# Optimization experiments

Hardware: AMD Instinct MI355X
Metric: run time of the kernel (lower is better)

## Reference

```python
import jax, jax.numpy as jnp
import numpy as np

HIDDEN = 2048
N_HEADS = 32
N_KV_HEADS = 8
N_GROUPS = N_HEADS // N_KV_HEADS  # 4
HEAD_DIM = HIDDEN // N_HEADS      # 64
BATCH, SEQ = 2, 2048


def setup_inputs() -> dict:
    key = jax.random.key(0)
    ks = jax.random.split(key, 5)
    s = 0.02
    return {
        "x": jax.random.normal(ks[0], (BATCH, SEQ, HIDDEN), dtype=jnp.float32),
        "Wq": jax.random.normal(ks[1], (HIDDEN, HIDDEN), dtype=jnp.float32) * s,
        "Wk": jax.random.normal(ks[2], (N_KV_HEADS * HEAD_DIM, HIDDEN), dtype=jnp.float32) * s,
        "Wv": jax.random.normal(ks[3], (N_KV_HEADS * HEAD_DIM, HIDDEN), dtype=jnp.float32) * s,
        "Wo": jax.random.normal(ks[4], (HIDDEN, HIDDEN), dtype=jnp.float32) * s,
    }


def reference(x, Wq, Wk, Wv, Wo):
    b, s, _ = x.shape
    # Projections (nn.Linear: y = x @ W.T)
    q = (x @ Wq.T).reshape(b, s, N_KV_HEADS, N_GROUPS, HEAD_DIM)  # group heads by kv head
    k = (x @ Wk.T).reshape(b, s, N_KV_HEADS, HEAD_DIM)
    v = (x @ Wv.T).reshape(b, s, N_KV_HEADS, HEAD_DIM)
    scale = 1.0 / jnp.sqrt(jnp.asarray(HEAD_DIM, dtype=x.dtype))
    # Grouped scores: equivalent to repeat_interleave of K over groups
    scores = jnp.einsum('bqhgd,bkhd->bhgqk', q, k) * scale  # [b, kvh, g, s, s]
    causal_mask = jnp.triu(jnp.ones((s, s), dtype=bool), k=1)
    scores = jnp.where(causal_mask, -jnp.inf, scores)
    attn = jax.nn.softmax(scores, axis=-1)
    out = jnp.einsum('bhgqk,bkhd->bqhgd', attn, v)  # [b, s, kvh, g, hd]
    out = out.reshape(b, s, HIDDEN)
    return out @ Wo.T
```

## Files before the change

### kernel.cpp

```cpp
#include <hip/hip_runtime.h>

#define HIDDEN 2048
#define NHEADS 32
#define NKV 8
#define HD 64
#define BATCH 2
#define SEQ 2048
#define MROWS (BATCH*SEQ)
#define KVDIM (NKV*HD)
#define QKVN (HIDDEN + 2*KVDIM)

typedef __bf16 bf16x8 __attribute__((ext_vector_type(8)));
typedef __bf16 bf16x4 __attribute__((ext_vector_type(4)));
typedef float f32x4 __attribute__((ext_vector_type(4)));

__device__ inline f32x4 mfma32(bf16x8 a, bf16x8 b, f32x4 c) {
    return __builtin_amdgcn_mfma_f32_16x16x32_bf16(a, b, c, 0, 0, 0);
}

__device__ inline void gld16(const __bf16* g, __bf16* l) {
    __builtin_amdgcn_global_load_lds((const __attribute__((address_space(1))) void*)g,
                                     (__attribute__((address_space(3))) void*)l, 16, 0, 0);
}

__global__ __launch_bounds__(256) void cast_all(const float* __restrict__ x,
                                                const float* __restrict__ wq,
                                                const float* __restrict__ wk,
                                                const float* __restrict__ wv,
                                                const float* __restrict__ wo,
                                                __bf16* __restrict__ xb,
                                                __bf16* __restrict__ wqkv,
                                                __bf16* __restrict__ wob,
                                                float qscale) {
    int blk = blockIdx.x;
    const float* src; __bf16* dst; float sc = 1.0f; size_t off;
    if (blk < 8192)        { src = x;  dst = xb;   off = (size_t)blk * 1024; }
    else if (blk < 12288)  { src = wq; dst = wqkv; off = (size_t)(blk - 8192) * 1024; sc = qscale; }
    else if (blk < 13312)  { src = wk; dst = wqkv + (size_t)HIDDEN * HIDDEN; off = (size_t)(blk - 12288) * 1024; }
    else if (blk < 14336)  { src = wv; dst = wqkv + (size_t)(HIDDEN + KVDIM) * HIDDEN; off = (size_t)(blk - 13312) * 1024; }
    else                   { src = wo; dst = wob;  off = (size_t)(blk - 14336) * 1024; }
    size_t i4 = off + (size_t)threadIdx.x * 4;
    float4 f = *(const float4*)(src + i4);
    dst[i4 + 0] = (__bf16)(f.x * sc);
    dst[i4 + 1] = (__bf16)(f.y * sc);
    dst[i4 + 2] = (__bf16)(f.z * sc);
    dst[i4 + 3] = (__bf16)(f.w * sc);
}

__device__ inline void store_val(__bf16* C, size_t idx, float v) { C[idx] = (__bf16)v; }
__device__ inline void store_val(float* C, size_t idx, float v) { C[idx] = v; }

template <typename OutT>
__global__ __launch_bounds__(256) void gemm128(const __bf16* __restrict__ A,
                                               const __bf16* __restrict__ B,
                                               OutT* __restrict__ C,
                                               int M, int N, int K) {
    __shared__ __bf16 As[2][128][32];
    __shared__ __bf16 Bs[2][128][32];
    const int tid  = threadIdx.x;
    const int lane = tid & 63;
    const int w    = tid >> 6;
    const int col  = lane & 15;
    const int quad = lane >> 4;
    const int m0 = blockIdx.y * 128;
    const int n0 = blockIdx.x * 128;
    const int wm = (w >> 1) * 64;
    const int wn = (w & 1) * 64;

    f32x4 acc[4][4];
    #pragma unroll
    for (int i = 0; i < 4; i++)
        #pragma unroll
        for (int j = 0; j < 4; j++) acc[i][j] = (f32x4){0.f,0.f,0.f,0.f};

    const int lrow = lane >> 2;
    const int lcol = (lane & 3) * 8;

    auto stage = [&](int k0, int buf) {
        #pragma unroll
        for (int c = 0; c < 4; c++) {
            int chunk = w * 4 + c;
            if (chunk < 8) {
                const __bf16* g = A + (size_t)(m0 + chunk*16 + lrow) * K + k0 + lcol;
                gld16(g, &As[buf][chunk*16][0]);
            } else {
                int bc = chunk - 8;
                const __bf16* g = B + (size_t)(n0 + bc*16 + lrow) * K + k0 + lcol;
                gld16(g, &Bs[buf][bc*16][0]);
            }
        }
    };

    const int nk = K / 32;
    stage(0, 0);
    for (int ki = 0; ki < nk; ki++) {
        const int buf = ki & 1;
        __syncthreads();
        if (ki + 1 < nk) stage((ki + 1) * 32, buf ^ 1);

        bf16x8 af[4], bfr[4];
        #pragma unroll
        for (int i = 0; i < 4; i++) af[i]  = *(const bf16x8*)&As[buf][wm + i*16 + col][quad*8];
        #pragma unroll
        for (int j = 0; j < 4; j++) bfr[j] = *(const bf16x8*)&Bs[buf][wn + j*16 + col][quad*8];
        #pragma unroll
        for (int i = 0; i < 4; i++)
            #pragma unroll
            for (int j = 0; j < 4; j++)
                acc[i][j] = __builtin_amdgcn_mfma_f32_16x16x32_bf16(af[i], bfr[j], acc[i][j], 0, 0, 0);
    }

    #pragma unroll
    for (int i = 0; i < 4; i++) {
        #pragma unroll
        for (int r = 0; r < 4; r++) {
            int mrow = m0 + wm + i*16 + quad*4 + r;
            size_t base = (size_t)mrow * N + n0 + wn;
            #pragma unroll
            for (int j = 0; j < 4; j++)
                store_val(C, base + j*16 + col, acc[i][j][r]);
        }
    }
}

__global__ __launch_bounds__(512, 2) void gemm256(const __bf16* __restrict__ A,
                                                  const __bf16* __restrict__ B,
                                                  __bf16* __restrict__ C,
                                                  int M, int N, int K) {
    __shared__ __bf16 As[2][256][64];
    __shared__ __bf16 Bs[2][192][64];
    const int tid  = threadIdx.x;
    const int lane = tid & 63;
    const int w    = tid >> 6;
    const int wr   = w >> 2;
    const int wc   = w & 3;
    const int col  = lane & 15;
    const int quad = lane >> 4;
    const int m0 = blockIdx.y * 256;
    const int n0 = blockIdx.x * 192;
    const int nk = K >> 6;

    f32x4 acc[8][3];
    #pragma unroll
    for (int i = 0; i < 8; i++)
        #pragma unroll
        for (int j = 0; j < 3; j++) acc[i][j] = (f32x4){0.f,0.f,0.f,0.f};

    bf16x8 amh0[4][2];
    bf16x8 amh1[4][2];
    bf16x8 b01[2][2];
    bf16x8 b2v[2];

    const int r8 = lane >> 3, c8 = lane & 7;
    const __bf16* pA0 = A + (size_t)(m0 + w*16 +     r8) * K + ((c8 ^ quad) * 8);
    const __bf16* pA1 = A + (size_t)(m0 + w*16 + 8 + r8) * K + ((c8 ^ (4 + quad)) * 8);
    const __bf16* pB  = B + (size_t)(n0 + w*8 +      r8) * K + ((c8 ^ ((w & 1) * 4 + quad)) * 8);
    const int rsw = col >> 1;

    auto issue = [&](int tt) {
        if (tt < nk) {
            int b = tt & 1; size_t ko = (size_t)tt * 64;
            gld16(pA0 + ko,                  &As[b][w*16][0]);
            gld16(pA1 + ko,                  &As[b][w*16 + 8][0]);
            gld16(pA0 + (size_t)128*K + ko,  &As[b][128 + w*16][0]);
            gld16(pA1 + (size_t)128*K + ko,  &As[b][128 + w*16 + 8][0]);
            gld16(pB + ko,                   &Bs[b][w*8][0]);
            gld16(pB + (size_t)64*K + ko,    &Bs[b][64 + w*8][0]);
            gld16(pB + (size_t)128*K + ko,   &Bs[b][128 + w*8][0]);
        }
    };
    auto rdA = [&](bf16x8 (&dst)[4][2], int b, int rowbase) {
        #pragma unroll
        for (int i = 0; i < 4; i++) {
            const __bf16* rp = &As[b][rowbase + i*16 + col][0];
            #pragma unroll
            for (int kk = 0; kk < 2; kk++)
                dst[i][kk] = *(const bf16x8*)(rp + (((kk*4 + quad) ^ rsw) * 8));
        }
    };
    auto rdB01 = [&](int b) {
        #pragma unroll
        for (int j = 0; j < 2; j++) {
            const __bf16* rp = &Bs[b][wc*48 + j*16 + col][0];
            #pragma unroll
            for (int kk = 0; kk < 2; kk++)
                b01[j][kk] = *(const bf16x8*)(rp + (((kk*4 + quad) ^ rsw) * 8));
        }
    };

    issue(0); issue(1);
    __asm__ volatile("s_waitcnt vmcnt(7)" ::: "memory");
    __builtin_amdgcn_s_barrier();
    __asm__ volatile("" ::: "memory");
    rdA(amh0, 0, wr*128);
    rdB01(0);

    for (int t = 0; t < nk; ++t) {
        const int buf = t & 1;
        {
            const __bf16* rp = &Bs[buf][wc*48 + 32 + col][0];
            #pragma unroll
            for (int kk = 0; kk < 2; kk++)
                b2v[kk] = *(const bf16x8*)(rp + (((kk*4 + quad) ^ rsw) * 8));
        }
        __builtin_amdgcn_s_setprio(1);
        #pragma unroll
        for (int i = 0; i < 4; i++)
            #pragma unroll
            for (int j = 0; j < 2; j++)
                #pragma unroll
                for (int kk = 0; kk < 2; kk++)
                    acc[i][j] = mfma32(amh0[i][kk], b01[j][kk], acc[i][j]);
        __builtin_amdgcn_s_setprio(0);
        rdA(amh1, buf, wr*128 + 64);
        __builtin_amdgcn_s_setprio(1);
        #pragma unroll
        for (int i = 0; i < 4; i++)
            #pragma unroll
            for (int kk = 0; kk < 2; kk++)
                acc[i][2] = mfma32(amh0[i][kk], b2v[kk], acc[i][2]);
        __builtin_amdgcn_s_setprio(0);
        __builtin_amdgcn_s_setprio(1);
        #pragma unroll
        for (int i = 0; i < 4; i++)
            #pragma unroll
            for (int j = 0; j < 2; j++)
                #pragma unroll
                for (int kk = 0; kk < 2; kk++)
                    acc[4+i][j] = mfma32(amh1[i][kk], b01[j][kk], acc[4+i][j]);
        __builtin_amdgcn_s_setprio(0);

        __asm__ volatile("s_waitcnt vmcnt(0) lgkmcnt(0)" ::: "memory");
        __builtin_amdgcn_sched_barrier(0);
        __builtin_amdgcn_s_barrier();
        __asm__ volatile("" ::: "memory");

        if (t + 1 < nk) {
            rdA(amh0, buf ^ 1, wr*128);
            rdB01(buf ^ 1);
        }
        issue(t + 2);

        __builtin_amdgcn_s_setprio(1);
        #pragma unroll
        for (int i = 0; i < 4; i++)
            #pragma unroll
            for (int kk = 0; kk < 2; kk++)
                acc[4+i][2] = mfma32(amh1[i][kk], b2v[kk], acc[4+i][2]);
        __builtin_amdgcn_s_setprio(0);
    }

    #pragma unroll
    for (int i16 = 0; i16 < 8; i16++) {
        #pragma unroll
        for (int r = 0; r < 4; r++) {
            size_t base = (size_t)(m0 + wr*128 + i16*16 + quad*4 + r) * N + n0 + wc*48;
            #pragma unroll
            for (int j = 0; j < 3; j++)
                C[base + j*16 + col] = (__bf16)acc[i16][j][r];
        }
    }
}

__global__ __launch_bounds__(256) void transpose_v(const __bf16* __restrict__ QKV,
                                                   __bf16* __restrict__ VT) {
    __shared__ __bf16 tile[64][72];
    const int r0 = blockIdx.x * 64;
    const int s0 = blockIdx.y * 64;
    const int t  = threadIdx.x;
    #pragma unroll
    for (int cc = 0; cc < 2; cc++) {
        int c = t + cc * 256;
        int i = c >> 3;
        int j8 = (c & 7) * 8;
        bf16x8 v = *(const bf16x8*)(QKV + (size_t)(s0 + i) * QKVN + (HIDDEN + KVDIM) + r0 + j8);
        *(bf16x8*)&tile[i][j8] = v;
    }
    __syncthreads();
    #pragma unroll
    for (int cc = 0; cc < 2; cc++) {
        int c = t + cc * 256;
        int d = c >> 3;
        int m = c & 7;
        bf16x8 vv;
        #pragma unroll
        for (int tt = 0; tt < 8; tt++) {
            int sl = (m >> 2) * 32 + (tt >> 2) * 16 + (m & 3) * 4 + (tt & 3);
            vv[tt] = tile[sl][d];
        }
        *(bf16x8*)(VT + (size_t)(r0 + d) * MROWS + s0 + m * 8) = vv;
    }
}

__global__ __launch_bounds__(256) void flash_attn(const __bf16* __restrict__ QKV,
                                                  const __bf16* __restrict__ VT,
                                                  __bf16* __restrict__ O) {
    const int bid  = blockIdx.x;
    const int t    = 31 - (bid >> 6);
    const int head = (bid >> 1) & 31;
    const int b    = bid & 1;
    const int kvh  = head >> 2;
    const int tid  = threadIdx.x;
    const int lane = tid & 63;
    const int w    = tid >> 6;
    const int col  = lane & 15;
    const int quad = lane >> 4;

    const int qb   = t * 64 + w * 16;
    const int n32  = (t + 1) * 2;

    __shared__ __bf16 Ks[3][2][32][32];
    __shared__ __bf16 Vs[3][64][32];

    const size_t qO = (size_t)(b * SEQ + qb + col) * QKVN + head * HD;
    bf16x8 aq0 = *(const bf16x8*)(QKV + qO + quad * 8);
    bf16x8 aq1 = *(const bf16x8*)(QKV + qO + 32 + quad * 8);

    bf16x8 ones8;
    #pragma unroll
    for (int j = 0; j < 8; j++) ones8[j] = (__bf16)1.0f;

    f32x4 o[4];
    #pragma unroll
    for (int dn = 0; dn < 4; dn++) o[dn] = (f32x4){0.f,0.f,0.f,0.f};
    f32x4 lsum = (f32x4){0.f,0.f,0.f,0.f};

    const int lrow = lane >> 2;
    const int srcc8 = (((lane & 3) ^ (lrow & 3)) * 8);
    const int swz   = (quad ^ (col & 3)) * 8;
    const size_t bS = (size_t)b * SEQ;

    const __bf16 *g0, *g1;
    size_t gstep;
    if (w < 2) {
        g0 = QKV + (bS + lrow) * QKVN + HIDDEN + kvh * HD + w * 32 + srcc8;
        g1 = g0 + (size_t)16 * QKVN;
        gstep = (size_t)32 * QKVN;
    } else {
        g0 = VT + (size_t)(kvh * HD + (w - 2) * 32 + lrow) * MROWS + bS + (lane & 3) * 8;
        g1 = g0 + (size_t)16 * MROWS;
        gstep = 32;
    }

    auto stage = [&](int sb) {
        if (w < 2) {
            gld16(g0, &Ks[sb][w][0][0]);
            gld16(g1, &Ks[sb][w][16][0]);
        } else {
            gld16(g0, &Vs[sb][(w - 2) * 32][0]);
            gld16(g1, &Vs[sb][(w - 2) * 32 + 16][0]);
        }
        g0 += gstep; g1 += gstep;
    };

    stage(0);
    stage(1);
    int cur = 0, nx2 = 2;
    for (int kt = 0; kt < n32; kt++) {
        const int kbase = kt * 32;
        if (kt + 1 < n32) { __asm__ volatile("s_waitcnt vmcnt(2)" ::: "memory"); }
        else              { __asm__ volatile("s_waitcnt vmcnt(0)" ::: "memory"); }
        __builtin_amdgcn_s_barrier();
        __asm__ volatile("" ::: "memory");
        if (kt + 2 < n32) stage(nx2);

        f32x4 s[2];
        s[0] = (f32x4){0.f,0.f,0.f,0.f};
        s[1] = (f32x4){0.f,0.f,0.f,0.f};
        __builtin_amdgcn_s_setprio(1);
        #pragma unroll
        for (int j = 0; j < 2; j++) {
            bf16x8 bk0 = *(const bf16x8*)&Ks[cur][0][j*16 + col][swz];
            bf16x8 bk1 = *(const bf16x8*)&Ks[cur][1][j*16 + col][swz];
            s[j] = mfma32(bk0, aq0, s[j]);
            s[j] = mfma32(bk1, aq1, s[j]);
        }
        __builtin_amdgcn_s_setprio(0);

        if (kt >= n32 - 2) {
            #pragma unroll
            for (int j = 0; j < 2; j++)
                #pragma unroll
                for (int r = 0; r < 4; r++)
                    if (kbase + j*16 + quad*4 + r > qb + col) s[j][r] = -1e30f;
        }

        bf16x8 pa;
        #pragma unroll
        for (int j = 0; j < 2; j++)
            #pragma unroll
            for (int r = 0; r < 4; r++)
                pa[j*4 + r] = (__bf16)__builtin_amdgcn_exp2f(s[j][r]);

        __builtin_amdgcn_s_setprio(1);
        lsum = mfma32(pa, ones8, lsum);
        #pragma unroll
        for (int dn = 0; dn < 4; dn++) {
            bf16x8 bv = *(const bf16x8*)&Vs[cur][dn*16 + col][quad*8];
            o[dn] = mfma32(pa, bv, o[dn]);
        }
        __builtin_amdgcn_s_setprio(0);

        cur = (cur == 2) ? 0 : cur + 1;
        nx2 = (nx2 == 2) ? 0 : nx2 + 1;
    }

    #pragma unroll
    for (int r = 0; r < 4; r++) {
        float inv = 1.0f / lsum[r];
        __bf16* op = O + (size_t)(b * SEQ + qb + quad*4 + r) * HIDDEN + head * HD;
        #pragma unroll
        for (int dn = 0; dn < 4; dn++)
            op[dn*16 + col] = (__bf16)(o[dn][r] * inv);
    }
}

extern "C" void kernel_launch(void* const* d_in, const int* in_sizes, int n_in,
                              void* d_out, int out_size, void* d_ws, size_t ws_size,
                              hipStream_t stream) {
    const float* x  = (const float*)d_in[0];
    const float* Wq = (const float*)d_in[1];
    const float* Wk = (const float*)d_in[2];
    const float* Wv = (const float*)d_in[3];
    const float* Wo = (const float*)d_in[4];
    float* out = (float*)d_out;

    __bf16* p    = (__bf16*)d_ws;
    __bf16* xb   = p; p += (size_t)MROWS * HIDDEN;
    __bf16* wqkv = p; p += (size_t)QKVN * HIDDEN;
    __bf16* wob  = p; p += (size_t)HIDDEN * HIDDEN;
    __bf16* qkv  = p; p += (size_t)MROWS * QKVN;
    __bf16* vt   = p; p += (size_t)KVDIM * MROWS;
    __bf16* aob  = xb;

    const float qscale = 0.125f * 1.4426950408889634f;
    cast_all<<<18432, 256, 0, stream>>>(x, Wq, Wk, Wv, Wo, xb, wqkv, wob, qscale);

    gemm256<<<dim3(QKVN/192, MROWS/256), 512, 0, stream>>>(xb, wqkv, qkv, MROWS, QKVN, HIDDEN);
    transpose_v<<<dim3(KVDIM/64, MROWS/64), dim3(256), 0, stream>>>(qkv, vt);
    flash_attn<<<BATCH * NHEADS * (SEQ/64), dim3(256), 0, stream>>>(qkv, vt, aob);
    gemm128<float><<<dim3(HIDDEN/128, MROWS/128), dim3(256), 0, stream>>>(aob, wob, out, MROWS, HIDDEN, HIDDEN);
}
```

Baseline: 271.7 us.

## Double flash-attention query tile to 128 rows with two 16-row subtiles per wave

Each attention block now handles 128 query rows, and each wave computes two 16-row query subtiles against every K/V tile it stages in LDS. This halves the number of blocks and roughly halves the K/V global-to-LDS traffic per query row. A wave skips the MFMA work for its first subtile once that subtile lies entirely under the causal mask. The block-to-tile mapping is reordered to interleave heavy and light causal tiles, and the V tile now uses the same XOR swizzle as K. The cost is more registers per wave and fewer blocks, which may lower occupancy and tail balance.

Result: no change. 275.2 us (+1.3%).

```diff
diff --git a/kernel.cpp b/kernel.cpp
--- a/kernel.cpp
+++ b/kernel.cpp
@@ -296,7 +296,8 @@
                                                   const __bf16* __restrict__ VT,
                                                   __bf16* __restrict__ O) {
     const int bid  = blockIdx.x;
-    const int t    = 31 - (bid >> 6);
+    const int g    = bid >> 6;
+    const int t    = ((g >> 2) & 1) ? ((g & 8) ? (g - 12) : (g + 4)) : (15 - g);
     const int head = (bid >> 1) & 31;
     const int b    = bid & 1;
     const int kvh  = head >> 2;
@@ -306,24 +307,28 @@
     const int col  = lane & 15;
     const int quad = lane >> 4;
 
-    const int qb   = t * 64 + w * 16;
-    const int n32  = (t + 1) * 2;
+    const int qb   = t * 128 + w * 32;
+    const int n32  = (t + 1) * 4;
 
     __shared__ __bf16 Ks[3][2][32][32];
     __shared__ __bf16 Vs[3][64][32];
 
-    const size_t qO = (size_t)(b * SEQ + qb + col) * QKVN + head * HD;
-    bf16x8 aq0 = *(const bf16x8*)(QKV + qO + quad * 8);
-    bf16x8 aq1 = *(const bf16x8*)(QKV + qO + 32 + quad * 8);
+    const size_t qOA = (size_t)(b * SEQ + qb + col) * QKVN + head * HD;
+    const size_t qOB = qOA + (size_t)16 * QKVN;
+    bf16x8 aqA0 = *(const bf16x8*)(QKV + qOA + quad * 8);
+    bf16x8 aqA1 = *(const bf16x8*)(QKV + qOA + 32 + quad * 8);
+    bf16x8 aqB0 = *(const bf16x8*)(QKV + qOB + quad * 8);
+    bf16x8 aqB1 = *(const bf16x8*)(QKV + qOB + 32 + quad * 8);
 
     bf16x8 ones8;
     #pragma unroll
     for (int j = 0; j < 8; j++) ones8[j] = (__bf16)1.0f;
 
-    f32x4 o[4];
-    #pragma unroll
-    for (int dn = 0; dn < 4; dn++) o[dn] = (f32x4){0.f,0.f,0.f,0.f};
-    f32x4 lsum = (f32x4){0.f,0.f,0.f,0.f};
+    f32x4 oA[4], oB[4];
+    #pragma unroll
+    for (int dn = 0; dn < 4; dn++) { oA[dn] = (f32x4){0.f,0.f,0.f,0.f}; oB[dn] = (f32x4){0.f,0.f,0.f,0.f}; }
+    f32x4 lsumA = (f32x4){0.f,0.f,0.f,0.f};
+    f32x4 lsumB = (f32x4){0.f,0.f,0.f,0.f};
 
     const int lrow = lane >> 2;
     const int srcc8 = (((lane & 3) ^ (lrow & 3)) * 8);
@@ -337,7 +342,7 @@
         g1 = g0 + (size_t)16 * QKVN;
         gstep = (size_t)32 * QKVN;
     } else {
-        g0 = VT + (size_t)(kvh * HD + (w - 2) * 32 + lrow) * MROWS + bS + (lane & 3) * 8;
+        g0 = VT + (size_t)(kvh * HD + (w - 2) * 32 + lrow) * MROWS + bS + srcc8;
         g1 = g0 + (size_t)16 * MROWS;
         gstep = 32;
     }
@@ -364,42 +369,67 @@
         __asm__ volatile("" ::: "memory");
         if (kt + 2 < n32) stage(nx2);
 
-        f32x4 s[2];
-        s[0] = (f32x4){0.f,0.f,0.f,0.f};
-        s[1] = (f32x4){0.f,0.f,0.f,0.f};
-        __builtin_amdgcn_s_setprio(1);
-        #pragma unroll
-        for (int j = 0; j < 2; j++) {
-            bf16x8 bk0 = *(const bf16x8*)&Ks[cur][0][j*16 + col][swz];
-            bf16x8 bk1 = *(const bf16x8*)&Ks[cur][1][j*16 + col][swz];
-            s[j] = mfma32(bk0, aq0, s[j]);
-            s[j] = mfma32(bk1, aq1, s[j]);
-        }
-        __builtin_amdgcn_s_setprio(0);
-
-        if (kt >= n32 - 2) {
+        const bool doB = (kbase <= qb + 31);
+        const bool doA = (kbase <= qb + 15);
+
+        if (doB) {
+            f32x4 sA[2], sB[2];
+            #pragma unroll
+            for (int j = 0; j < 2; j++) { sA[j] = (f32x4){0.f,0.f,0.f,0.f}; sB[j] = (f32x4){0.f,0.f,0.f,0.f}; }
+            __builtin_amdgcn_s_setprio(1);
+            #pragma unroll
+            for (int j = 0; j < 2; j++) {
+                bf16x8 bk0 = *(const bf16x8*)&Ks[cur][0][j*16 + col][swz];
+                bf16x8 bk1 = *(const bf16x8*)&Ks[cur][1][j*16 + col][swz];
+                sB[j] = mfma32(bk0, aqB0, sB[j]);
+                sB[j] = mfma32(bk1, aqB1, sB[j]);
+                if (doA) {
+                    sA[j] = mfma32(bk0, aqA0, sA[j]);
+                    sA[j] = mfma32(bk1, aqA1, sA[j]);
+                }
+            }
+            __builtin_amdgcn_s_setprio(0);
+
+            if (kbase + 31 > qb + 16) {
+                #pragma unroll
+                for (int j = 0; j < 2; j++)
+                    #pragma unroll
+                    for (int r = 0; r < 4; r++)
+                        if (kbase + j*16 + quad*4 + r > qb + 16 + col) sB[j][r] = -1e30f;
+            }
+            if (doA && (kbase + 31 > qb)) {
+                #pragma unroll
+                for (int j = 0; j < 2; j++)
+                    #pragma unroll
+                    for (int r = 0; r < 4; r++)
+                        if (kbase + j*16 + quad*4 + r > qb + col) sA[j][r] = -1e30f;
+            }
+
+            bf16x8 paB, paA;
             #pragma unroll
             for (int j = 0; j < 2; j++)
                 #pragma unroll
                 for (int r = 0; r < 4; r++)
-                    if (kbase + j*16 + quad*4 + r > qb + col) s[j][r] = -1e30f;
-        }
-
-        bf16x8 pa;
-        #pragma unroll
-        for (int j = 0; j < 2; j++)
-            #pragma unroll
-            for (int r = 0; r < 4; r++)
-                pa[j*4 + r] = (__bf16)__builtin_amdgcn_exp2f(s[j][r]);
-
-        __builtin_amdgcn_s_setprio(1);
-        lsum = mfma32(pa, ones8, lsum);
-        #pragma unroll
-        for (int dn = 0; dn < 4; dn++) {
-            bf16x8 bv = *(const bf16x8*)&Vs[cur][dn*16 + col][quad*8];
-            o[dn] = mfma32(pa, bv, o[dn]);
-        }
-        __builtin_amdgcn_s_setprio(0);
+                    paB[j*4 + r] = (__bf16)__builtin_amdgcn_exp2f(sB[j][r]);
+            if (doA) {
+                #pragma unroll
+                for (int j = 0; j < 2; j++)
+                    #pragma unroll
+                    for (int r = 0; r < 4; r++)
+                        paA[j*4 + r] = (__bf16)__builtin_amdgcn_exp2f(sA[j][r]);
+            }
+
+            __builtin_amdgcn_s_setprio(1);
+            lsumB = mfma32(paB, ones8, lsumB);
+            if (doA) lsumA = mfma32(paA, ones8, lsumA);
+            #pragma unroll
+            for (int dn = 0; dn < 4; dn++) {
+                bf16x8 bv = *(const bf16x8*)&Vs[cur][dn*16 + col][swz];
+                oB[dn] = mfma32(paB, bv, oB[dn]);
+                if (doA) oA[dn] = mfma32(paA, bv, oA[dn]);
+            }
+            __builtin_amdgcn_s_setprio(0);
+        }
 
         cur = (cur == 2) ? 0 : cur + 1;
         nx2 = (nx2 == 2) ? 0 : nx2 + 1;
@@ -407,11 +437,15 @@
 
     #pragma unroll
     for (int r = 0; r < 4; r++) {
-        float inv = 1.0f / lsum[r];
-        __bf16* op = O + (size_t)(b * SEQ + qb + quad*4 + r) * HIDDEN + head * HD;
-        #pragma unroll
-        for (int dn = 0; dn < 4; dn++)
-            op[dn*16 + col] = (__bf16)(o[dn][r] * inv);
+        float invA = 1.0f / lsumA[r];
+        float invB = 1.0f / lsumB[r];
+        __bf16* opA = O + (size_t)(b * SEQ + qb + quad*4 + r) * HIDDEN + head * HD;
+        __bf16* opB = O + (size_t)(b * SEQ + qb + 16 + quad*4 + r) * HIDDEN + head * HD;
+        #pragma unroll
+        for (int dn = 0; dn < 4; dn++) {
+            opA[dn*16 + col] = (__bf16)(oA[dn][r] * invA);
+            opB[dn*16 + col] = (__bf16)(oB[dn][r] * invB);
+        }
     }
 }
 
@@ -438,6 +472,6 @@
 
     gemm256<<<dim3(QKVN/192, MROWS/256), 512, 0, stream>>>(xb, wqkv, qkv, MROWS, QKVN, HIDDEN);
     transpose_v<<<dim3(KVDIM/64, MROWS/64), dim3(256), 0, stream>>>(qkv, vt);
-    flash_attn<<<BATCH * NHEADS * (SEQ/64), dim3(256), 0, stream>>>(qkv, vt, aob);
+    flash_attn<<<BATCH * NHEADS * (SEQ/128), dim3(256), 0, stream>>>(qkv, vt, aob);
     gemm128<float><<<dim3(HIDDEN/128, MROWS/128), dim3(256), 0, stream>>>(aob, wob, out, MROWS, HIDDEN, HIDDEN);
 }
```
